# Optimization experiments

Measured on AMD Instinct MI355X. Metric: run time of the kernel, lower is better.

## Reference

```python
import jax, jax.numpy as jnp
import numpy as np

N = 50000
E = 800000
D_IN = 128
D_HID = 128
D_OUT = 64


def setup_inputs() -> dict:
    key = jax.random.key(0)
    ks = jax.random.split(key, 9)
    x = jax.random.normal(ks[0], (N, D_IN), dtype=jnp.float32)
    edge_index = jax.random.randint(ks[1], (2, E), 0, N, dtype=jnp.int64)
    # PyG SAGEConv params: lin_l (neighbor path, with bias), lin_r (root path, no bias)
    s1 = 1.0 / np.sqrt(D_IN)
    s2 = 1.0 / np.sqrt(D_HID)
    return {
        "x": x,
        "edge_index": edge_index,
        "W1l": jax.random.uniform(ks[2], (D_IN, D_HID), jnp.float32, -s1, s1),
        "b1": jax.random.uniform(ks[3], (D_HID,), jnp.float32, -s1, s1),
        "W1r": jax.random.uniform(ks[4], (D_IN, D_HID), jnp.float32, -s1, s1),
        "W2l": jax.random.uniform(ks[5], (D_HID, D_OUT), jnp.float32, -s2, s2),
        "b2": jax.random.uniform(ks[6], (D_OUT,), jnp.float32, -s2, s2),
        "W2r": jax.random.uniform(ks[7], (D_HID, D_OUT), jnp.float32, -s2, s2),
    }


def _sage_conv(h, src, dst, Wl, b, Wr, n_nodes):
    # mean-aggregate source features onto target nodes
    msg = h[src]  # [E, d] gather
    summed = jax.ops.segment_sum(msg, dst, num_segments=n_nodes)
    cnt = jax.ops.segment_sum(jnp.ones((src.shape[0],), h.dtype), dst, num_segments=n_nodes)
    mean = summed / jnp.maximum(cnt, 1.0)[:, None]
    return mean @ Wl + b + h @ Wr


def reference(x, edge_index, W1l, b1, W1r, W2l, b2, W2r):
    src, dst = edge_index[0], edge_index[1]
    n = x.shape[0]
    h = jax.nn.relu(_sage_conv(x, src, dst, W1l, b1, W1r, n))
    # dropout is identity in eval mode
    return _sage_conv(h, src, dst, W2l, b2, W2r, n)
```

## Files before the change

### kernel.cpp

```cpp
#include <hip/hip_runtime.h>

#define NN   50000
#define NE   800000
#define CAP  48
#define NPG  6250
#define EPB  3125
#define SEG  576

#define BIN_BLOCKS  256
#define ZERO_BLOCKS 196
#define SCAT_BLOCKS 2048
#define CVT_BLOCKS  (3125 + 128)

typedef __attribute__((ext_vector_type(8))) short bf16x8;
typedef __attribute__((ext_vector_type(4))) unsigned short u16x4;
typedef __attribute__((ext_vector_type(4))) float f32x4;

__device__ __forceinline__ unsigned short f2b(float f) {
    unsigned int u = __builtin_bit_cast(unsigned int, f);
    u += 0x7FFFu + ((u >> 16) & 1u);
    return (unsigned short)(u >> 16);
}
__device__ __forceinline__ float b2f_lo(unsigned int u) {
    return __builtin_bit_cast(float, u << 16);
}
__device__ __forceinline__ float b2f_hi(unsigned int u) {
    return __builtin_bit_cast(float, u & 0xFFFF0000u);
}

__global__ __launch_bounds__(256) void prep_kernel(const int* __restrict__ src,
                                                   const int* __restrict__ dst,
                                                   int* __restrict__ bcnt,
                                                   unsigned* __restrict__ stage,
                                                   int* __restrict__ cursor) {
    if (blockIdx.x < BIN_BLOCKS) {
        __shared__ int cnt[16][8];
        __shared__ int repoff[16][8];
        const int tid = threadIdx.x;
        const int b   = blockIdx.x;
        const int r   = tid >> 4;
        if (tid < 128) ((int*)cnt)[tid] = 0;
        __syncthreads();

        unsigned recs[13], metas[13];
#pragma unroll
        for (int it = 0; it < 13; ++it) {
            const int i = it * 256 + tid;
            metas[it] = 0xFFFFFFFFu;
            if (i < EPB) {
                const int e = b * EPB + i;
                const int s = src[e], d = dst[e];
                const int g = d / NPG;
                const int dloc = d - g * NPG;
                const int slot = atomicAdd(&cnt[r][g], 1);
                recs[it]  = ((unsigned)dloc << 16) | (unsigned)s;
                metas[it] = ((unsigned)r << 20) | ((unsigned)g << 16) | (unsigned)slot;
            }
        }
        __syncthreads();
        if (tid < 8) {
            int off = 0;
#pragma unroll
            for (int rr = 0; rr < 16; ++rr) { repoff[rr][tid] = off; off += cnt[rr][tid]; }
            bcnt[tid * 256 + b] = off;
        }
        __syncthreads();
#pragma unroll
        for (int it = 0; it < 13; ++it) {
            if (metas[it] != 0xFFFFFFFFu) {
                const int rr   = metas[it] >> 20;
                const int g    = (metas[it] >> 16) & 7;
                const int slot = metas[it] & 0xFFFF;
                const int pos  = repoff[rr][g] + slot;
                if (pos < SEG) stage[((g << 8) + b) * SEG + pos] = recs[it];
            }
        }
    } else {
        int i = (blockIdx.x - BIN_BLOCKS) * 256 + threadIdx.x;
        if (i < NN) cursor[i] = 0;
    }
}

__global__ __launch_bounds__(256) void scatter_kernel(const int* __restrict__ bcnt,
                                                      const unsigned* __restrict__ stage,
                                                      int* __restrict__ cursor,
                                                      unsigned short* __restrict__ col,
                                                      const float* __restrict__ x,
                                                      const float* __restrict__ W1l,
                                                      const float* __restrict__ W1r,
                                                      const float* __restrict__ W2l,
                                                      const float* __restrict__ W2r,
                                                      unsigned short* __restrict__ xb,
                                                      unsigned short* __restrict__ Bt1,
                                                      unsigned short* __restrict__ Bt2) {
    if (blockIdx.x < SCAT_BLOCKS) {
        const int g = blockIdx.x & 7;
        const int b = blockIdx.x >> 3;
        int cnt = bcnt[g * 256 + b];
        if (cnt > SEG) cnt = SEG;
        const unsigned* sp = stage + (size_t)((g << 8) + b) * SEG;
        const int n0 = g * NPG;
        for (int i = threadIdx.x; i < cnt; i += 256) {
            unsigned rec = sp[i];
            int d = n0 + (int)(rec >> 16);
            int p = atomicAdd(&cursor[d], 1);
            if (p < CAP) col[d * CAP + p] = (unsigned short)(rec & 0xFFFFu);
        }
    } else if (blockIdx.x < SCAT_BLOCKS + 3125) {
        int i = (blockIdx.x - SCAT_BLOCKS) * 256 + threadIdx.x;
        const float4* p = reinterpret_cast<const float4*>(x) + (size_t)i * 2;
        float4 a = p[0], b = p[1];
        uint4 u;
        u.x = (unsigned)f2b(a.x) | ((unsigned)f2b(a.y) << 16);
        u.y = (unsigned)f2b(a.z) | ((unsigned)f2b(a.w) << 16);
        u.z = (unsigned)f2b(b.x) | ((unsigned)f2b(b.y) << 16);
        u.w = (unsigned)f2b(b.z) | ((unsigned)f2b(b.w) << 16);
        reinterpret_cast<uint4*>(xb)[i] = u;
    } else {
        int t = (blockIdx.x - SCAT_BLOCKS - 3125) * 256 + threadIdx.x;
        if (t < 32768) {
            int c = t >> 8, k = t & 255;
            float v = (k < 128) ? W1l[k * 128 + c] : W1r[(k - 128) * 128 + c];
            Bt1[c * 256 + k] = f2b(v);
        }
        if (t < 16384) {
            int c = t >> 7, k = t & 127;
            float v = (c < 64) ? W2l[k * 64 + c] : W2r[k * 64 + (c - 64)];
            Bt2[c * 128 + k] = f2b(v);
        }
    }
}

__global__ __launch_bounds__(256) void agg_gemm12(const unsigned short* __restrict__ xb,
                                                  const int* __restrict__ cursor,
                                                  const unsigned short* __restrict__ col,
                                                  const unsigned short* __restrict__ Bt1,
                                                  const unsigned short* __restrict__ Bt2,
                                                  const float* __restrict__ b1,
                                                  unsigned short* __restrict__ hlb,
                                                  unsigned short* __restrict__ hrb) {
    constexpr int LDA = 264;
    constexpr int LDH = 136;
    __shared__ unsigned short As[64 * LDA];

    const int base = blockIdx.x * 64;
    const int tid  = threadIdx.x;
    const int l    = tid & 15;
    const int sub  = tid >> 4;

    const uint4* fp = reinterpret_cast<const uint4*>(xb);

    for (int gq = 0; gq < 4; ++gq) {
        const int r  = gq * 16 + sub;
        const int gn = base + r;
        float a0 = 0.f, a1 = 0.f, a2 = 0.f, a3 = 0.f,
              a4 = 0.f, a5 = 0.f, a6 = 0.f, a7 = 0.f;
        uint4 xrow = make_uint4(0, 0, 0, 0);
        if (gn < NN) {
            int len = cursor[gn];
            len = (len > CAP) ? CAP : len;
            const unsigned short* cl = col + gn * CAP;
            int j = 0;
            for (; j + 4 <= len; j += 4) {
                u16x4 c4 = *reinterpret_cast<const u16x4*>(cl + j);
                uint4 v0 = fp[(int)c4[0] * 16 + l];
                uint4 v1 = fp[(int)c4[1] * 16 + l];
                uint4 v2 = fp[(int)c4[2] * 16 + l];
                uint4 v3 = fp[(int)c4[3] * 16 + l];
                a0 += (b2f_lo(v0.x) + b2f_lo(v1.x)) + (b2f_lo(v2.x) + b2f_lo(v3.x));
                a1 += (b2f_hi(v0.x) + b2f_hi(v1.x)) + (b2f_hi(v2.x) + b2f_hi(v3.x));
                a2 += (b2f_lo(v0.y) + b2f_lo(v1.y)) + (b2f_lo(v2.y) + b2f_lo(v3.y));
                a3 += (b2f_hi(v0.y) + b2f_hi(v1.y)) + (b2f_hi(v2.y) + b2f_hi(v3.y));
                a4 += (b2f_lo(v0.z) + b2f_lo(v1.z)) + (b2f_lo(v2.z) + b2f_lo(v3.z));
                a5 += (b2f_hi(v0.z) + b2f_hi(v1.z)) + (b2f_hi(v2.z) + b2f_hi(v3.z));
                a6 += (b2f_lo(v0.w) + b2f_lo(v1.w)) + (b2f_lo(v2.w) + b2f_lo(v3.w));
                a7 += (b2f_hi(v0.w) + b2f_hi(v1.w)) + (b2f_hi(v2.w) + b2f_hi(v3.w));
            }
            for (; j < len; ++j) {
                uint4 v0 = fp[(int)cl[j] * 16 + l];
                a0 += b2f_lo(v0.x);  a1 += b2f_hi(v0.x);
                a2 += b2f_lo(v0.y);  a3 += b2f_hi(v0.y);
                a4 += b2f_lo(v0.z);  a5 += b2f_hi(v0.z);
                a6 += b2f_lo(v0.w);  a7 += b2f_hi(v0.w);
            }
            const float inv = 1.0f / fmaxf((float)len, 1.0f);
            a0 *= inv; a1 *= inv; a2 *= inv; a3 *= inv;
            a4 *= inv; a5 *= inv; a6 *= inv; a7 *= inv;
            xrow = fp[gn * 16 + l];
        }
        uint4 u;
        u.x = (unsigned)f2b(a0) | ((unsigned)f2b(a1) << 16);
        u.y = (unsigned)f2b(a2) | ((unsigned)f2b(a3) << 16);
        u.z = (unsigned)f2b(a4) | ((unsigned)f2b(a5) << 16);
        u.w = (unsigned)f2b(a6) | ((unsigned)f2b(a7) << 16);
        *reinterpret_cast<uint4*>(&As[r * LDA + l * 8])       = u;
        *reinterpret_cast<uint4*>(&As[r * LDA + 128 + l * 8]) = xrow;
    }
    __syncthreads();

    const int wid  = tid >> 6, lane = tid & 63;
    const int lr   = lane & 15;
    const int lk   = (lane >> 4) * 8;
    const int ccol = lane & 15;
    const int ri   = (lane >> 4) * 4;

    f32x4 acc[4][2];
#pragma unroll
    for (int t = 0; t < 4; ++t) {
        acc[t][0] = (f32x4){0.f, 0.f, 0.f, 0.f};
        acc[t][1] = (f32x4){0.f, 0.f, 0.f, 0.f};
    }
    for (int ks = 0; ks < 8; ++ks) {
        const int k = ks * 32 + lk;
        bf16x8 b0 = *reinterpret_cast<const bf16x8*>(Bt1 + (size_t)(wid * 32 + lr) * 256 + k);
        bf16x8 b1 = *reinterpret_cast<const bf16x8*>(Bt1 + (size_t)(wid * 32 + 16 + lr) * 256 + k);
#pragma unroll
        for (int t = 0; t < 4; ++t) {
            bf16x8 a = *reinterpret_cast<const bf16x8*>(&As[(t * 16 + lr) * LDA + k]);
            acc[t][0] = __builtin_amdgcn_mfma_f32_16x16x32_bf16(a, b0, acc[t][0], 0, 0, 0);
            acc[t][1] = __builtin_amdgcn_mfma_f32_16x16x32_bf16(a, b1, acc[t][1], 0, 0, 0);
        }
    }
    __syncthreads();

    unsigned short* Hs = As;
#pragma unroll
    for (int t = 0; t < 4; ++t) {
#pragma unroll
        for (int f = 0; f < 2; ++f) {
            const int colg = wid * 32 + f * 16 + ccol;
            const float bv = b1[colg];
#pragma unroll
            for (int i = 0; i < 4; ++i) {
                Hs[(t * 16 + ri + i) * LDH + colg] = f2b(fmaxf(acc[t][f][i] + bv, 0.f));
            }
        }
    }
    __syncthreads();

    f32x4 acc2[4][2];
#pragma unroll
    for (int t = 0; t < 4; ++t) {
        acc2[t][0] = (f32x4){0.f, 0.f, 0.f, 0.f};
        acc2[t][1] = (f32x4){0.f, 0.f, 0.f, 0.f};
    }
    for (int ks = 0; ks < 4; ++ks) {
        const int k = ks * 32 + lk;
        bf16x8 b0 = *reinterpret_cast<const bf16x8*>(Bt2 + (size_t)(wid * 32 + lr) * 128 + k);
        bf16x8 b1 = *reinterpret_cast<const bf16x8*>(Bt2 + (size_t)(wid * 32 + 16 + lr) * 128 + k);
#pragma unroll
        for (int t = 0; t < 4; ++t) {
            bf16x8 a = *reinterpret_cast<const bf16x8*>(&Hs[(t * 16 + lr) * LDH + k]);
            acc2[t][0] = __builtin_amdgcn_mfma_f32_16x16x32_bf16(a, b0, acc2[t][0], 0, 0, 0);
            acc2[t][1] = __builtin_amdgcn_mfma_f32_16x16x32_bf16(a, b1, acc2[t][1], 0, 0, 0);
        }
    }

#pragma unroll
    for (int t = 0; t < 4; ++t) {
#pragma unroll
        for (int f = 0; f < 2; ++f) {
            const int colg = wid * 32 + f * 16 + ccol;
#pragma unroll
            for (int i = 0; i < 4; ++i) {
                const int gn = base + t * 16 + ri + i;
                if (gn < NN) {
                    float v = acc2[t][f][i];
                    if (colg < 64) hlb[(size_t)gn * 64 + colg] = f2b(v);
                    else           hrb[(size_t)gn * 64 + (colg - 64)] = f2b(v);
                }
            }
        }
    }
}

__global__ __launch_bounds__(256) void agg2_kernel(const unsigned short* __restrict__ feat,
                                                   const int* __restrict__ cursor,
                                                   const unsigned short* __restrict__ col,
                                                   const unsigned short* __restrict__ hrb,
                                                   const float* __restrict__ b2,
                                                   float* __restrict__ outf) {
    const int n = blockIdx.x * 32 + (threadIdx.x >> 3);
    const int l = threadIdx.x & 7;
    if (n >= NN) return;
    int len = cursor[n];
    len = (len > CAP) ? CAP : len;
    float a0 = 0.f, a1 = 0.f, a2 = 0.f, a3 = 0.f, a4 = 0.f, a5 = 0.f, a6 = 0.f, a7 = 0.f;
    const uint4* fp = reinterpret_cast<const uint4*>(feat);
    const unsigned short* cl = col + n * CAP;

    int j = 0;
    for (; j + 4 <= len; j += 4) {
        u16x4 c4 = *reinterpret_cast<const u16x4*>(cl + j);
        uint4 v0 = fp[(int)c4[0] * 8 + l];
        uint4 v1 = fp[(int)c4[1] * 8 + l];
        uint4 v2 = fp[(int)c4[2] * 8 + l];
        uint4 v3 = fp[(int)c4[3] * 8 + l];
        a0 += (b2f_lo(v0.x) + b2f_lo(v1.x)) + (b2f_lo(v2.x) + b2f_lo(v3.x));
        a1 += (b2f_hi(v0.x) + b2f_hi(v1.x)) + (b2f_hi(v2.x) + b2f_hi(v3.x));
        a2 += (b2f_lo(v0.y) + b2f_lo(v1.y)) + (b2f_lo(v2.y) + b2f_lo(v3.y));
        a3 += (b2f_hi(v0.y) + b2f_hi(v1.y)) + (b2f_hi(v2.y) + b2f_hi(v3.y));
        a4 += (b2f_lo(v0.z) + b2f_lo(v1.z)) + (b2f_lo(v2.z) + b2f_lo(v3.z));
        a5 += (b2f_hi(v0.z) + b2f_hi(v1.z)) + (b2f_hi(v2.z) + b2f_hi(v3.z));
        a6 += (b2f_lo(v0.w) + b2f_lo(v1.w)) + (b2f_lo(v2.w) + b2f_lo(v3.w));
        a7 += (b2f_hi(v0.w) + b2f_hi(v1.w)) + (b2f_hi(v2.w) + b2f_hi(v3.w));
    }
    for (; j < len; ++j) {
        uint4 v0 = fp[(int)cl[j] * 8 + l];
        a0 += b2f_lo(v0.x);  a1 += b2f_hi(v0.x);
        a2 += b2f_lo(v0.y);  a3 += b2f_hi(v0.y);
        a4 += b2f_lo(v0.z);  a5 += b2f_hi(v0.z);
        a6 += b2f_lo(v0.w);  a7 += b2f_hi(v0.w);
    }
    const float inv = 1.0f / fmaxf((float)len, 1.0f);
    uint4 hv = reinterpret_cast<const uint4*>(hrb)[(size_t)n * 8 + l];
    const float4* bp = reinterpret_cast<const float4*>(b2 + l * 8);
    float4 bv0 = bp[0], bv1 = bp[1];
    float4 o0 = make_float4(a0 * inv + b2f_lo(hv.x) + bv0.x,
                            a1 * inv + b2f_hi(hv.x) + bv0.y,
                            a2 * inv + b2f_lo(hv.y) + bv0.z,
                            a3 * inv + b2f_hi(hv.y) + bv0.w);
    float4 o1 = make_float4(a4 * inv + b2f_lo(hv.z) + bv1.x,
                            a5 * inv + b2f_hi(hv.z) + bv1.y,
                            a6 * inv + b2f_lo(hv.w) + bv1.z,
                            a7 * inv + b2f_hi(hv.w) + bv1.w);
    float4* op = reinterpret_cast<float4*>(outf + (size_t)n * 64) + l * 2;
    op[0] = o0; op[1] = o1;
}

extern "C" void kernel_launch(void* const* d_in, const int* in_sizes, int n_in,
                              void* d_out, int out_size, void* d_ws, size_t ws_size,
                              hipStream_t stream) {
    const float* x   = (const float*)d_in[0];
    const int*   ei  = (const int*)d_in[1];
    const float* W1l = (const float*)d_in[2];
    const float* b1  = (const float*)d_in[3];
    const float* W1r = (const float*)d_in[4];
    const float* W2l = (const float*)d_in[5];
    const float* b2  = (const float*)d_in[6];
    const float* W2r = (const float*)d_in[7];

    const int* src = ei;
    const int* dst = ei + NE;

    char* ws = (char*)d_ws;
    int* cursor = (int*)ws;
    int* bcnt   = (int*)(ws + 200000);
    unsigned short* col = (unsigned short*)(ws + 208384);
    unsigned short* xb  = (unsigned short*)(ws + 9808384);
    unsigned short* hlb = (unsigned short*)(ws + 22608384);
    unsigned short* hrb = (unsigned short*)(ws + 29008384);
    unsigned*       stage = (unsigned*)(ws + 35408384);
    unsigned short* Bt1 = (unsigned short*)(ws + 48208384);
    unsigned short* Bt2 = (unsigned short*)(ws + 48273920);
    float* outp = (float*)d_out;

    prep_kernel<<<BIN_BLOCKS + ZERO_BLOCKS, 256, 0, stream>>>(src, dst, bcnt, stage,
                                                              cursor);
    scatter_kernel<<<SCAT_BLOCKS + CVT_BLOCKS, 256, 0, stream>>>(
        bcnt, stage, cursor, col, x, W1l, W1r, W2l, W2r, xb, Bt1, Bt2);

    agg_gemm12<<<(NN + 63) / 64, 256, 0, stream>>>(xb, cursor, col, Bt1, Bt2,
                                                   b1, hlb, hrb);

    agg2_kernel<<<(NN + 31) / 32, 256, 0, stream>>>(hlb, cursor, col, hrb, b2, outp);
}
```

Baseline: 114.4 us.

## Split layer-1 aggregation into feature-sliced gather kernel and separate GEMM

```diff
diff --git a/kernel.cpp b/kernel.cpp
--- a/kernel.cpp
+++ b/kernel.cpp
@@ -11,6 +11,7 @@
 #define ZERO_BLOCKS 196
 #define SCAT_BLOCKS 2048
 #define CVT_BLOCKS  (3125 + 128)
+#define AGG1_CHUNKS 391
 
 typedef __attribute__((ext_vector_type(8))) short bf16x8;
 typedef __attribute__((ext_vector_type(4))) unsigned short u16x4;
@@ -91,6 +92,7 @@
                                                       const float* __restrict__ W2l,
                                                       const float* __restrict__ W2r,
                                                       unsigned short* __restrict__ xb,
+                                                      unsigned short* __restrict__ xbs,
                                                       unsigned short* __restrict__ Bt1,
                                                       unsigned short* __restrict__ Bt2) {
     if (blockIdx.x < SCAT_BLOCKS) {
@@ -116,6 +118,8 @@
         u.z = (unsigned)f2b(b.x) | ((unsigned)f2b(b.y) << 16);
         u.w = (unsigned)f2b(b.z) | ((unsigned)f2b(b.w) << 16);
         reinterpret_cast<uint4*>(xb)[i] = u;
+        const int n = i >> 4, sub = i & 15;
+        reinterpret_cast<uint4*>(xbs)[((sub >> 1) * NN + n) * 2 + (sub & 1)] = u;
     } else {
         int t = (blockIdx.x - SCAT_BLOCKS - 3125) * 256 + threadIdx.x;
         if (t < 32768) {
@@ -131,70 +135,77 @@
     }
 }
 
-__global__ __launch_bounds__(256) void agg_gemm12(const unsigned short* __restrict__ xb,
-                                                  const int* __restrict__ cursor,
-                                                  const unsigned short* __restrict__ col,
-                                                  const unsigned short* __restrict__ Bt1,
-                                                  const unsigned short* __restrict__ Bt2,
-                                                  const float* __restrict__ b1,
-                                                  unsigned short* __restrict__ hlb,
-                                                  unsigned short* __restrict__ hrb) {
+__global__ __launch_bounds__(256) void agg1s_kernel(const unsigned short* __restrict__ xbs,
+                                                    const int* __restrict__ cursor,
+                                                    const unsigned short* __restrict__ col,
+                                                    unsigned short* __restrict__ m1) {
+    const int g    = blockIdx.x & 7;
+    const int node = (blockIdx.x >> 3) * 128 + ((int)threadIdx.x >> 1);
+    const int half = threadIdx.x & 1;
+    if (node >= NN) return;
+    int len = cursor[node];
+    len = (len > CAP) ? CAP : len;
+    const unsigned short* cl = col + node * CAP;
+    const uint4* fp = reinterpret_cast<const uint4*>(xbs) + (size_t)g * NN * 2 + half;
+
+    float a0 = 0.f, a1 = 0.f, a2 = 0.f, a3 = 0.f, a4 = 0.f, a5 = 0.f, a6 = 0.f, a7 = 0.f;
+    int j = 0;
+    for (; j + 4 <= len; j += 4) {
+        u16x4 c4 = *reinterpret_cast<const u16x4*>(cl + j);
+        uint4 v0 = fp[(int)c4[0] * 2];
+        uint4 v1 = fp[(int)c4[1] * 2];
+        uint4 v2 = fp[(int)c4[2] * 2];
+        uint4 v3 = fp[(int)c4[3] * 2];
+        a0 += (b2f_lo(v0.x) + b2f_lo(v1.x)) + (b2f_lo(v2.x) + b2f_lo(v3.x));
+        a1 += (b2f_hi(v0.x) + b2f_hi(v1.x)) + (b2f_hi(v2.x) + b2f_hi(v3.x));
+        a2 += (b2f_lo(v0.y) + b2f_lo(v1.y)) + (b2f_lo(v2.y) + b2f_lo(v3.y));
+        a3 += (b2f_hi(v0.y) + b2f_hi(v1.y)) + (b2f_hi(v2.y) + b2f_hi(v3.y));
+        a4 += (b2f_lo(v0.z) + b2f_lo(v1.z)) + (b2f_lo(v2.z) + b2f_lo(v3.z));
+        a5 += (b2f_hi(v0.z) + b2f_hi(v1.z)) + (b2f_hi(v2.z) + b2f_hi(v3.z));
+        a6 += (b2f_lo(v0.w) + b2f_lo(v1.w)) + (b2f_lo(v2.w) + b2f_lo(v3.w));
+        a7 += (b2f_hi(v0.w) + b2f_hi(v1.w)) + (b2f_hi(v2.w) + b2f_hi(v3.w));
+    }
+    for (; j < len; ++j) {
+        uint4 v0 = fp[(int)cl[j] * 2];
+        a0 += b2f_lo(v0.x);  a1 += b2f_hi(v0.x);
+        a2 += b2f_lo(v0.y);  a3 += b2f_hi(v0.y);
+        a4 += b2f_lo(v0.z);  a5 += b2f_hi(v0.z);
+        a6 += b2f_lo(v0.w);  a7 += b2f_hi(v0.w);
+    }
+    const float inv = 1.0f / fmaxf((float)len, 1.0f);
+    a0 *= inv; a1 *= inv; a2 *= inv; a3 *= inv;
+    a4 *= inv; a5 *= inv; a6 *= inv; a7 *= inv;
+    uint4 u;
+    u.x = (unsigned)f2b(a0) | ((unsigned)f2b(a1) << 16);
+    u.y = (unsigned)f2b(a2) | ((unsigned)f2b(a3) << 16);
+    u.z = (unsigned)f2b(a4) | ((unsigned)f2b(a5) << 16);
+    u.w = (unsigned)f2b(a6) | ((unsigned)f2b(a7) << 16);
+    reinterpret_cast<uint4*>(m1)[(size_t)node * 16 + g * 2 + half] = u;
+}
+
+__global__ __launch_bounds__(256) void gemm12_kernel(const unsigned short* __restrict__ m1,
+                                                     const unsigned short* __restrict__ xb,
+                                                     const unsigned short* __restrict__ Bt1,
+                                                     const unsigned short* __restrict__ Bt2,
+                                                     const float* __restrict__ b1,
+                                                     unsigned short* __restrict__ hlb,
+                                                     unsigned short* __restrict__ hrb) {
     constexpr int LDA = 264;
     constexpr int LDH = 136;
     __shared__ unsigned short As[64 * LDA];
 
     const int base = blockIdx.x * 64;
     const int tid  = threadIdx.x;
-    const int l    = tid & 15;
-    const int sub  = tid >> 4;
-
-    const uint4* fp = reinterpret_cast<const uint4*>(xb);
-
-    for (int gq = 0; gq < 4; ++gq) {
-        const int r  = gq * 16 + sub;
-        const int gn = base + r;
-        float a0 = 0.f, a1 = 0.f, a2 = 0.f, a3 = 0.f,
-              a4 = 0.f, a5 = 0.f, a6 = 0.f, a7 = 0.f;
-        uint4 xrow = make_uint4(0, 0, 0, 0);
+
+    for (int idx = tid; idx < 64 * 32; idx += 256) {
+        int r = idx >> 5, c = idx & 31;
+        int gn = base + r;
+        uint4 v = make_uint4(0, 0, 0, 0);
         if (gn < NN) {
-            int len = cursor[gn];
-            len = (len > CAP) ? CAP : len;
-            const unsigned short* cl = col + gn * CAP;
-            int j = 0;
-            for (; j + 4 <= len; j += 4) {
-                u16x4 c4 = *reinterpret_cast<const u16x4*>(cl + j);
-                uint4 v0 = fp[(int)c4[0] * 16 + l];
-                uint4 v1 = fp[(int)c4[1] * 16 + l];
-                uint4 v2 = fp[(int)c4[2] * 16 + l];
-                uint4 v3 = fp[(int)c4[3] * 16 + l];
-                a0 += (b2f_lo(v0.x) + b2f_lo(v1.x)) + (b2f_lo(v2.x) + b2f_lo(v3.x));
-                a1 += (b2f_hi(v0.x) + b2f_hi(v1.x)) + (b2f_hi(v2.x) + b2f_hi(v3.x));
-                a2 += (b2f_lo(v0.y) + b2f_lo(v1.y)) + (b2f_lo(v2.y) + b2f_lo(v3.y));
-                a3 += (b2f_hi(v0.y) + b2f_hi(v1.y)) + (b2f_hi(v2.y) + b2f_hi(v3.y));
-                a4 += (b2f_lo(v0.z) + b2f_lo(v1.z)) + (b2f_lo(v2.z) + b2f_lo(v3.z));
-                a5 += (b2f_hi(v0.z) + b2f_hi(v1.z)) + (b2f_hi(v2.z) + b2f_hi(v3.z));
-                a6 += (b2f_lo(v0.w) + b2f_lo(v1.w)) + (b2f_lo(v2.w) + b2f_lo(v3.w));
-                a7 += (b2f_hi(v0.w) + b2f_hi(v1.w)) + (b2f_hi(v2.w) + b2f_hi(v3.w));
-            }
-            for (; j < len; ++j) {
-                uint4 v0 = fp[(int)cl[j] * 16 + l];
-                a0 += b2f_lo(v0.x);  a1 += b2f_hi(v0.x);
-                a2 += b2f_lo(v0.y);  a3 += b2f_hi(v0.y);
-                a4 += b2f_lo(v0.z);  a5 += b2f_hi(v0.z);
-                a6 += b2f_lo(v0.w);  a7 += b2f_hi(v0.w);
-            }
-            const float inv = 1.0f / fmaxf((float)len, 1.0f);
-            a0 *= inv; a1 *= inv; a2 *= inv; a3 *= inv;
-            a4 *= inv; a5 *= inv; a6 *= inv; a7 *= inv;
-            xrow = fp[gn * 16 + l];
-        }
-        uint4 u;
-        u.x = (unsigned)f2b(a0) | ((unsigned)f2b(a1) << 16);
-        u.y = (unsigned)f2b(a2) | ((unsigned)f2b(a3) << 16);
-        u.z = (unsigned)f2b(a4) | ((unsigned)f2b(a5) << 16);
-        u.w = (unsigned)f2b(a6) | ((unsigned)f2b(a7) << 16);
-        *reinterpret_cast<uint4*>(&As[r * LDA + l * 8])       = u;
-        *reinterpret_cast<uint4*>(&As[r * LDA + 128 + l * 8]) = xrow;
+            v = (c < 16) ? reinterpret_cast<const uint4*>(m1)[(size_t)gn * 16 + c]
+                         : reinterpret_cast<const uint4*>(xb)[(size_t)gn * 16 + (c - 16)];
+        }
+        *reinterpret_cast<uint4*>(&As[r * LDA + c * 8]) = v;
     }
     __syncthreads();
 
@@ -213,12 +224,12 @@
     for (int ks = 0; ks < 8; ++ks) {
         const int k = ks * 32 + lk;
         bf16x8 b0 = *reinterpret_cast<const bf16x8*>(Bt1 + (size_t)(wid * 32 + lr) * 256 + k);
-        bf16x8 b1 = *reinterpret_cast<const bf16x8*>(Bt1 + (size_t)(wid * 32 + 16 + lr) * 256 + k);
+        bf16x8 b1v = *reinterpret_cast<const bf16x8*>(Bt1 + (size_t)(wid * 32 + 16 + lr) * 256 + k);
 #pragma unroll
         for (int t = 0; t < 4; ++t) {
             bf16x8 a = *reinterpret_cast<const bf16x8*>(&As[(t * 16 + lr) * LDA + k]);
             acc[t][0] = __builtin_amdgcn_mfma_f32_16x16x32_bf16(a, b0, acc[t][0], 0, 0, 0);
-            acc[t][1] = __builtin_amdgcn_mfma_f32_16x16x32_bf16(a, b1, acc[t][1], 0, 0, 0);
+            acc[t][1] = __builtin_amdgcn_mfma_f32_16x16x32_bf16(a, b1v, acc[t][1], 0, 0, 0);
         }
     }
     __syncthreads();
@@ -247,12 +258,12 @@
     for (int ks = 0; ks < 4; ++ks) {
         const int k = ks * 32 + lk;
         bf16x8 b0 = *reinterpret_cast<const bf16x8*>(Bt2 + (size_t)(wid * 32 + lr) * 128 + k);
-        bf16x8 b1 = *reinterpret_cast<const bf16x8*>(Bt2 + (size_t)(wid * 32 + 16 + lr) * 128 + k);
+        bf16x8 b1v = *reinterpret_cast<const bf16x8*>(Bt2 + (size_t)(wid * 32 + 16 + lr) * 128 + k);
 #pragma unroll
         for (int t = 0; t < 4; ++t) {
             bf16x8 a = *reinterpret_cast<const bf16x8*>(&Hs[(t * 16 + lr) * LDH + k]);
             acc2[t][0] = __builtin_amdgcn_mfma_f32_16x16x32_bf16(a, b0, acc2[t][0], 0, 0, 0);
-            acc2[t][1] = __builtin_amdgcn_mfma_f32_16x16x32_bf16(a, b1, acc2[t][1], 0, 0, 0);
+            acc2[t][1] = __builtin_amdgcn_mfma_f32_16x16x32_bf16(a, b1v, acc2[t][1], 0, 0, 0);
         }
     }
 
@@ -348,9 +359,11 @@
     int* bcnt   = (int*)(ws + 200000);
     unsigned short* col = (unsigned short*)(ws + 208384);
     unsigned short* xb  = (unsigned short*)(ws + 9808384);
+    unsigned short* xbs = (unsigned short*)(ws + 22608384);
     unsigned short* hlb = (unsigned short*)(ws + 22608384);
     unsigned short* hrb = (unsigned short*)(ws + 29008384);
     unsigned*       stage = (unsigned*)(ws + 35408384);
+    unsigned short* m1  = (unsigned short*)(ws + 35408384);
     unsigned short* Bt1 = (unsigned short*)(ws + 48208384);
     unsigned short* Bt2 = (unsigned short*)(ws + 48273920);
     float* outp = (float*)d_out;
@@ -358,10 +371,11 @@
     prep_kernel<<<BIN_BLOCKS + ZERO_BLOCKS, 256, 0, stream>>>(src, dst, bcnt, stage,
                                                               cursor);
     scatter_kernel<<<SCAT_BLOCKS + CVT_BLOCKS, 256, 0, stream>>>(
-        bcnt, stage, cursor, col, x, W1l, W1r, W2l, W2r, xb, Bt1, Bt2);
-
-    agg_gemm12<<<(NN + 63) / 64, 256, 0, stream>>>(xb, cursor, col, Bt1, Bt2,
-                                                   b1, hlb, hrb);
+        bcnt, stage, cursor, col, x, W1l, W1r, W2l, W2r, xb, xbs, Bt1, Bt2);
+
+    agg1s_kernel<<<8 * AGG1_CHUNKS, 256, 0, stream>>>(xbs, cursor, col, m1);
+
+    gemm12_kernel<<<(NN + 63) / 64, 256, 0, stream>>>(m1, xb, Bt1, Bt2, b1, hlb, hrb);
 
     agg2_kernel<<<(NN + 31) / 32, 256, 0, stream>>>(hlb, cursor, col, hrb, b2, outp);
 }
```

Result: slower. 134.1 us (+17.3%).
